# Kernel tuning notes

Hardware: AMD Instinct MI355X
Metric: run time of the kernel (lower is better)

The kernel has to match this reference:

```python
import jax, jax.numpy as jnp
import numpy as np

BN_EPS = 1e-5
COS_EPS = 1e-8


def _bn_train(x, gamma, beta):
    # BatchNorm1d in training mode: stats over (batch, length) per channel
    mean = jnp.mean(x, axis=(0, 2), keepdims=True)
    var = jnp.var(x, axis=(0, 2), keepdims=True)
    xn = (x - mean) * jax.lax.rsqrt(var + BN_EPS)
    return xn * gamma[None, :, None] + beta[None, :, None]


def _conv1d(x, w, pad):
    # x: [B, Cin, L], w: [Cout, Cin, K]
    return jax.lax.conv_general_dilated(
        x, w, window_strides=(1,), padding=[(pad, pad)],
        dimension_numbers=('NCH', 'OIH', 'NCH'))


def _spe_self_atten(h):
    # h: [B, c, L]; cosine-similarity attention over channels
    norms = jnp.sqrt(jnp.sum(h * h, axis=2))                 # [B, c]
    denom = jnp.maximum(norms[:, :, None] * norms[:, None, :], COS_EPS)
    sim = jnp.einsum('bcl,bdl->bcd', h, h) / denom            # [B, c, c]
    att = jax.nn.softmax(sim, axis=-1)
    return jnp.einsum('bcd,bdl->bcl', att, h) + h


def setup_inputs() -> dict:
    key = jax.random.key(0)
    ks = jax.random.split(key, 3)
    B, Cin, L = 256, 64, 2048
    planes, growth = 192, 48
    x = jax.random.normal(ks[0], (B, Cin, L), dtype=jnp.float32)
    W1 = jax.random.normal(ks[1], (planes, Cin, 1), dtype=jnp.float32) * (1.0 / np.sqrt(Cin))
    W2 = jax.random.normal(ks[2], (growth, planes, 3), dtype=jnp.float32) * (1.0 / np.sqrt(planes * 3))
    return {
        'x': x,
        'gamma1': jnp.ones((Cin,), jnp.float32),
        'beta1': jnp.zeros((Cin,), jnp.float32),
        'W1': W1,
        'gamma2': jnp.ones((planes,), jnp.float32),
        'beta2': jnp.zeros((planes,), jnp.float32),
        'W2': W2,
    }


def reference(x, gamma1, beta1, W1, gamma2, beta2, W2):
    out = jax.nn.relu(_bn_train(x, gamma1, beta1))
    out = _conv1d(out, W1, pad=0)
    out = jax.nn.relu(_bn_train(out, gamma2, beta2))
    out = _conv1d(out, W2, pad=1)
    out = _spe_self_atten(out)
    return jnp.concatenate((x, out), axis=1)
```

## Files before the change

### kernel.cpp

```cpp
#include <hip/hip_runtime.h>

#define BB 256
#define C0 64
#define LL 2048
#define PP 192
#define GG 48
#define CO 112
#define PBK 24
#define CBK 8

typedef float f32x4 __attribute__((ext_vector_type(4)));
typedef __bf16 bf16x8 __attribute__((ext_vector_type(8)));

static constexpr size_t OUT1_BYTES = (size_t)BB * PP * LL * 2;
static constexpr size_t H_BYTES    = (size_t)BB * GG * LL * 4;
static constexpr int    ZR_FLOATS  = 602624;

__device__ __forceinline__ float bflo(unsigned w) { return __uint_as_float(w << 16); }
__device__ __forceinline__ float bfhi(unsigned w) { return __uint_as_float(w & 0xffff0000u); }
__device__ __forceinline__ unsigned pk2bf(float a, float b) {
    unsigned ua = __float_as_uint(a); ua += 0x7fffu + ((ua >> 16) & 1u);
    unsigned ub = __float_as_uint(b); ub += 0x7fffu + ((ub >> 16) & 1u);
    return (ua >> 16) | (ub & 0xffff0000u);
}
__device__ __forceinline__ unsigned short f2bf(float f) {
    unsigned u = __float_as_uint(f); u += 0x7fffu + ((u >> 16) & 1u);
    return (unsigned short)(u >> 16);
}
__device__ __forceinline__ unsigned act2(unsigned w, float s0, float s1, float h0, float h1) {
    float y0 = fmaxf(fmaf(s0, bflo(w), h0), 0.f);
    float y1 = fmaxf(fmaf(s1, bfhi(w), h1), 0.f);
    return pk2bf(y0, y1);
}

__global__ void kp_pack(const float* __restrict__ W1, const float* __restrict__ W2,
                        unsigned short* __restrict__ W1p, unsigned short* __restrict__ W2p) {
    int i = blockIdx.x * 256 + threadIdx.x;
    if (i < PP * C0) W1p[i] = f2bf(W1[i]);
    if (i < 3 * GG * PP) {
        int tap = i / (GG * PP), r = i % (GG * PP);
        int g = r / PP, p = r % PP;
        W2p[i] = f2bf(W2[(g * PP + p) * 3 + tap]);
    }
}

__global__ __launch_bounds__(256) void k1_stats_copy_xT(
        const float* __restrict__ x, float* __restrict__ out, unsigned short* __restrict__ xT,
        float* __restrict__ bn1sum, float* __restrict__ bn1sq) {
    int b = blockIdx.x, lc = blockIdx.y, t = threadIdx.x;
    int c = t >> 2, li = t & 3;
    float s = 0.f, ss = 0.f;
    for (int q = 0; q < 16; ++q) {
        int l = lc * 256 + li * 64 + q * 4;
        float4 v = *(const float4*)&x[(size_t)(b * C0 + c) * LL + l];
        *(float4*)&out[(size_t)(b * CO + c) * LL + l] = v;
        s += v.x + v.y + v.z + v.w;
        ss += v.x * v.x + v.y * v.y + v.z * v.z + v.w * v.w;
        unsigned short* xp = &xT[(((size_t)(b * CBK + (c >> 3))) * LL + l) * 8 + (c & 7)];
        xp[0] = f2bf(v.x); xp[8] = f2bf(v.y); xp[16] = f2bf(v.z); xp[24] = f2bf(v.w);
    }
    s += __shfl_xor(s, 1); s += __shfl_xor(s, 2);
    ss += __shfl_xor(ss, 1); ss += __shfl_xor(ss, 2);
    if (li == 0) { atomicAdd(&bn1sum[c], s); atomicAdd(&bn1sq[c], ss); }
}

__global__ void k_bn_final(const float* __restrict__ sums, const float* __restrict__ sqs,
                           const float* __restrict__ gamma, const float* __restrict__ beta,
                           float* __restrict__ scale, float* __restrict__ shift,
                           int C, float invN) {
    int c = threadIdx.x;
    if (c < C) {
        float mean = sums[c] * invN;
        float var  = sqs[c] * invN - mean * mean;
        float r    = rsqrtf(var + 1e-5f);
        float sc   = gamma[c] * r;
        scale[c] = sc;
        shift[c] = beta[c] - mean * sc;
    }
}

__global__ __launch_bounds__(256, 2) void k2_conv1(
        const unsigned short* __restrict__ xT, const unsigned short* __restrict__ W1p,
        const float* __restrict__ par, unsigned short* __restrict__ out1) {
    int b = blockIdx.x, lt = blockIdx.y, t = threadIdx.x;
    int w = __builtin_amdgcn_readfirstlane(t >> 6);
    int lane = t & 63, lm = lane & 15, lg = lane >> 4;
    union AF { uint4 q; bf16x8 v; };
    AF afr[3][2];
    #pragma unroll
    for (int gf = 0; gf < 3; ++gf)
        #pragma unroll
        for (int kc = 0; kc < 2; ++kc)
            afr[gf][kc].q = *(const uint4*)&W1p[(w * 48 + gf * 16 + lm) * C0 + kc * 32 + lg * 8];
    f32x4 acc[3][8];
    #pragma unroll
    for (int gf = 0; gf < 3; ++gf)
        #pragma unroll
        for (int lf = 0; lf < 8; ++lf) acc[gf][lf] = f32x4{0.f, 0.f, 0.f, 0.f};
    int l0 = lt * 128;
    size_t xbase = (size_t)b * CBK * LL * 8;
    #pragma unroll
    for (int kc = 0; kc < 2; ++kc) {
        int cb = kc * 4 + lg;
        float4 sca = *(const float4*)&par[8 * cb];
        float4 scb = *(const float4*)&par[8 * cb + 4];
        float4 sha = *(const float4*)&par[64 + 8 * cb];
        float4 shb = *(const float4*)&par[64 + 8 * cb + 4];
        #pragma unroll
        for (int lf = 0; lf < 8; ++lf) {
            int l = l0 + lf * 16 + lm;
            uint4 q = *(const uint4*)&xT[xbase + ((size_t)cb * LL + l) * 8];
            union { uint4 q; bf16x8 v; } bf;
            bf.q.x = act2(q.x, sca.x, sca.y, sha.x, sha.y);
            bf.q.y = act2(q.y, sca.z, sca.w, sha.z, sha.w);
            bf.q.z = act2(q.z, scb.x, scb.y, shb.x, shb.y);
            bf.q.w = act2(q.w, scb.z, scb.w, shb.z, shb.w);
            #pragma unroll
            for (int gf = 0; gf < 3; ++gf)
                acc[gf][lf] = __builtin_amdgcn_mfma_f32_16x16x32_bf16(afr[gf][kc].v, bf.v, acc[gf][lf], 0, 0, 0);
        }
    }
    #pragma unroll
    for (int gf = 0; gf < 3; ++gf) {
        int g0 = w * 48 + gf * 16 + lg * 4;
        size_t obase = ((size_t)b * PBK + (g0 >> 3)) * LL * 8 + (g0 & 7);
        #pragma unroll
        for (int lf = 0; lf < 8; ++lf) {
            int l = l0 + lf * 16 + lm;
            uint2 pk;
            pk.x = pk2bf(acc[gf][lf][0], acc[gf][lf][1]);
            pk.y = pk2bf(acc[gf][lf][2], acc[gf][lf][3]);
            *(uint2*)&out1[obase + (size_t)l * 8] = pk;
        }
    }
}

__global__ __launch_bounds__(256) void k3_bn2_stats(
        const unsigned short* __restrict__ out1,
        float* __restrict__ bn2sum, float* __restrict__ bn2sq) {
    int pb = blockIdx.x, chunk = blockIdx.y, t = threadIdx.x;
    float s[8], ss[8];
    #pragma unroll
    for (int j = 0; j < 8; ++j) { s[j] = 0.f; ss[j] = 0.f; }
    for (int i = 0; i < 64; ++i) {
        int idx = chunk * 16384 + i * 256 + t;
        int b = idx >> 11, l = idx & 2047;
        uint4 q = *(const uint4*)&out1[(((size_t)(b * PBK + pb)) * LL + l) * 8];
        unsigned uu[4] = {q.x, q.y, q.z, q.w};
        #pragma unroll
        for (int j = 0; j < 4; ++j) {
            float f0 = bflo(uu[j]), f1 = bfhi(uu[j]);
            s[2 * j] += f0;      ss[2 * j] += f0 * f0;
            s[2 * j + 1] += f1;  ss[2 * j + 1] += f1 * f1;
        }
    }
    #pragma unroll
    for (int m = 1; m < 64; m <<= 1)
        #pragma unroll
        for (int j = 0; j < 8; ++j) { s[j] += __shfl_xor(s[j], m); ss[j] += __shfl_xor(ss[j], m); }
    if ((t & 63) == 0)
        #pragma unroll
        for (int j = 0; j < 8; ++j) {
            atomicAdd(&bn2sum[pb * 8 + j], s[j]);
            atomicAdd(&bn2sq[pb * 8 + j], ss[j]);
        }
}

__global__ __launch_bounds__(256, 2) void k4_conv2(
        const unsigned short* __restrict__ out1, const unsigned short* __restrict__ W2p,
        const float* __restrict__ par, float* __restrict__ h, float* __restrict__ norms2) {
    int b = blockIdx.x, lt = blockIdx.y, t = threadIdx.x;
    int w = __builtin_amdgcn_readfirstlane(t >> 6);
    int lane = t & 63, lm = lane & 15, lg = lane >> 4;
    int lb = lt * 128 + w * 32;
    f32x4 acc[3][2];
    #pragma unroll
    for (int gf = 0; gf < 3; ++gf) { acc[gf][0] = f32x4{0.f,0.f,0.f,0.f}; acc[gf][1] = f32x4{0.f,0.f,0.f,0.f}; }
    size_t obase = (size_t)b * PBK * LL * 8;
    for (int pc = 0; pc < 6; ++pc) {
        int pb = pc * 4 + lg;
        float4 sca = *(const float4*)&par[128 + 8 * pb];
        float4 scb = *(const float4*)&par[128 + 8 * pb + 4];
        float4 sha = *(const float4*)&par[320 + 8 * pb];
        float4 shb = *(const float4*)&par[320 + 8 * pb + 4];
        #pragma unroll
        for (int tap = 0; tap < 3; ++tap) {
            union AF { uint4 q; bf16x8 v; };
            AF afr[3];
            #pragma unroll
            for (int gf = 0; gf < 3; ++gf)
                afr[gf].q = *(const uint4*)&W2p[(tap * GG + gf * 16 + lm) * PP + pc * 32 + lg * 8];
            #pragma unroll
            for (int lf = 0; lf < 2; ++lf) {
                int lz = lb + lf * 16 + lm + tap - 1;
                union { uint4 q; bf16x8 v; } bf;
                if ((unsigned)lz < (unsigned)LL) {
                    uint4 q = *(const uint4*)&out1[obase + ((size_t)pb * LL + lz) * 8];
                    bf.q.x = act2(q.x, sca.x, sca.y, sha.x, sha.y);
                    bf.q.y = act2(q.y, sca.z, sca.w, sha.z, sha.w);
                    bf.q.z = act2(q.z, scb.x, scb.y, shb.x, shb.y);
                    bf.q.w = act2(q.w, scb.z, scb.w, shb.z, shb.w);
                } else {
                    bf.q = uint4{0u, 0u, 0u, 0u};
                }
                #pragma unroll
                for (int gf = 0; gf < 3; ++gf)
                    acc[gf][lf] = __builtin_amdgcn_mfma_f32_16x16x32_bf16(afr[gf].v, bf.v, acc[gf][lf], 0, 0, 0);
            }
        }
    }
    #pragma unroll
    for (int gf = 0; gf < 3; ++gf) {
        #pragma unroll
        for (int lf = 0; lf < 2; ++lf) {
            int l = lb + lf * 16 + lm;
            #pragma unroll
            for (int r = 0; r < 4; ++r) {
                int g = gf * 16 + lg * 4 + r;
                h[((size_t)(b * GG + g)) * LL + l] = acc[gf][lf][r];
            }
        }
        #pragma unroll
        for (int r = 0; r < 4; ++r) {
            float nv = acc[gf][0][r] * acc[gf][0][r] + acc[gf][1][r] * acc[gf][1][r];
            nv += __shfl_xor(nv, 1); nv += __shfl_xor(nv, 2);
            nv += __shfl_xor(nv, 4); nv += __shfl_xor(nv, 8);
            if (lm == 0) atomicAdd(&norms2[b * GG + gf * 16 + lg * 4 + r], nv);
        }
    }
}

__global__ __launch_bounds__(256) void k6_gram(
        const float* __restrict__ h, float* __restrict__ sim) {
    int b = blockIdx.x, ch = blockIdx.y, t = threadIdx.x;
    __shared__ float hl[GG * 260];
    int tr = t >> 4, tc = t & 15;
    float s00 = 0, s01 = 0, s02 = 0, s10 = 0, s11 = 0, s12 = 0, s20 = 0, s21 = 0, s22 = 0;
    for (int sub = 0; sub < 2; ++sub) {
        __syncthreads();
        for (int j = 0; j < 12; ++j) {
            int f = j * 256 + t;
            int r = f >> 6, lq = f & 63;
            float4 v = ((const float4*)h)[(size_t)(b * GG + r) * 512 + ch * 128 + sub * 64 + lq];
            *(float4*)&hl[r * 260 + lq * 4] = v;
        }
        __syncthreads();
        for (int l4 = 0; l4 < 64; ++l4) {
            float4 r0 = *(const float4*)&hl[(3 * tr + 0) * 260 + l4 * 4];
            float4 r1 = *(const float4*)&hl[(3 * tr + 1) * 260 + l4 * 4];
            float4 r2 = *(const float4*)&hl[(3 * tr + 2) * 260 + l4 * 4];
            float4 c0 = *(const float4*)&hl[(3 * tc + 0) * 260 + l4 * 4];
            float4 c1 = *(const float4*)&hl[(3 * tc + 1) * 260 + l4 * 4];
            float4 c2 = *(const float4*)&hl[(3 * tc + 2) * 260 + l4 * 4];
            s00 += r0.x * c0.x + r0.y * c0.y + r0.z * c0.z + r0.w * c0.w;
            s01 += r0.x * c1.x + r0.y * c1.y + r0.z * c1.z + r0.w * c1.w;
            s02 += r0.x * c2.x + r0.y * c2.y + r0.z * c2.z + r0.w * c2.w;
            s10 += r1.x * c0.x + r1.y * c0.y + r1.z * c0.z + r1.w * c0.w;
            s11 += r1.x * c1.x + r1.y * c1.y + r1.z * c1.z + r1.w * c1.w;
            s12 += r1.x * c2.x + r1.y * c2.y + r1.z * c2.z + r1.w * c2.w;
            s20 += r2.x * c0.x + r2.y * c0.y + r2.z * c0.z + r2.w * c0.w;
            s21 += r2.x * c1.x + r2.y * c1.y + r2.z * c1.z + r2.w * c1.w;
            s22 += r2.x * c2.x + r2.y * c2.y + r2.z * c2.z + r2.w * c2.w;
        }
    }
    float* sb = &sim[(size_t)b * 2304];
    atomicAdd(&sb[(3 * tr + 0) * 48 + 3 * tc + 0], s00);
    atomicAdd(&sb[(3 * tr + 0) * 48 + 3 * tc + 1], s01);
    atomicAdd(&sb[(3 * tr + 0) * 48 + 3 * tc + 2], s02);
    atomicAdd(&sb[(3 * tr + 1) * 48 + 3 * tc + 0], s10);
    atomicAdd(&sb[(3 * tr + 1) * 48 + 3 * tc + 1], s11);
    atomicAdd(&sb[(3 * tr + 1) * 48 + 3 * tc + 2], s12);
    atomicAdd(&sb[(3 * tr + 2) * 48 + 3 * tc + 0], s20);
    atomicAdd(&sb[(3 * tr + 2) * 48 + 3 * tc + 1], s21);
    atomicAdd(&sb[(3 * tr + 2) * 48 + 3 * tc + 2], s22);
}

__global__ __launch_bounds__(256) void k7_softmax_pv(
        const float* __restrict__ h, const float* __restrict__ sim,
        const float* __restrict__ norms2, float* __restrict__ out) {
    int b = blockIdx.x, ch = blockIdx.y, t = threadIdx.x;
    __shared__ float att[GG][GG];
    __shared__ float nrm[GG];
    if (t < GG) nrm[t] = sqrtf(norms2[b * GG + t]);
    __syncthreads();
    if (t < GG) {
        int r = t;
        const float* sr = &sim[(size_t)b * 2304 + r * 48];
        float nr = nrm[r];
        float m = -1e30f;
        for (int d = 0; d < GG; ++d) {
            float v = sr[d] / fmaxf(nr * nrm[d], 1e-8f);
            att[r][d] = v;
            m = fmaxf(m, v);
        }
        float ssum = 0.f;
        for (int d = 0; d < GG; ++d) {
            float e = __expf(att[r][d] - m);
            att[r][d] = e;
            ssum += e;
        }
        float inv = 1.f / ssum;
        for (int d = 0; d < GG; ++d) att[r][d] *= inv;
        att[r][r] += 1.0f;
    }
    __syncthreads();
    int l = ch * 512 + t;
    float h0[GG], h1[GG];
    #pragma unroll
    for (int d = 0; d < GG; ++d) {
        h0[d] = h[(size_t)(b * GG + d) * LL + l];
        h1[d] = h[(size_t)(b * GG + d) * LL + l + 256];
    }
    for (int c = 0; c < GG; ++c) {
        float a0 = 0.f, a1 = 0.f;
        #pragma unroll
        for (int dq = 0; dq < 12; ++dq) {
            float4 a4 = *(const float4*)&att[c][dq * 4];
            a0 += a4.x * h0[4 * dq] + a4.y * h0[4 * dq + 1] + a4.z * h0[4 * dq + 2] + a4.w * h0[4 * dq + 3];
            a1 += a4.x * h1[4 * dq] + a4.y * h1[4 * dq + 1] + a4.z * h1[4 * dq + 2] + a4.w * h1[4 * dq + 3];
        }
        out[(size_t)(b * CO + 64 + c) * LL + l] = a0;
        out[(size_t)(b * CO + 64 + c) * LL + l + 256] = a1;
    }
}

extern "C" void kernel_launch(void* const* d_in, const int* in_sizes, int n_in,
                              void* d_out, int out_size, void* d_ws, size_t ws_size,
                              hipStream_t stream) {
    const float* x      = (const float*)d_in[0];
    const float* gamma1 = (const float*)d_in[1];
    const float* beta1  = (const float*)d_in[2];
    const float* W1     = (const float*)d_in[3];
    const float* gamma2 = (const float*)d_in[4];
    const float* beta2  = (const float*)d_in[5];
    const float* W2     = (const float*)d_in[6];
    float* out = (float*)d_out;

    unsigned short* out1 = (unsigned short*)d_ws;
    float* h = (float*)((char*)d_ws + OUT1_BYTES);
    unsigned short* xT = (unsigned short*)h;
    float* zr  = (float*)((char*)d_ws + OUT1_BYTES + H_BYTES);
    float* par = zr + ZR_FLOATS;
    unsigned short* W1p = (unsigned short*)(par + 512);
    unsigned short* W2p = W1p + PP * C0;

    hipMemsetAsync(zr, 0, (size_t)ZR_FLOATS * sizeof(float), stream);

    const float invN = 1.0f / (float)((size_t)BB * LL);
    kp_pack<<<108, 256, 0, stream>>>(W1, W2, W1p, W2p);
    k1_stats_copy_xT<<<dim3(BB, 8), 256, 0, stream>>>(x, out, xT, zr + 0, zr + 64);
    k_bn_final<<<1, 64, 0, stream>>>(zr + 0, zr + 64, gamma1, beta1, par + 0, par + 64, 64, invN);
    k2_conv1<<<dim3(BB, 16), 256, 0, stream>>>(xT, W1p, par, out1);
    k3_bn2_stats<<<dim3(PBK, 32), 256, 0, stream>>>(out1, zr + 128, zr + 320);
    k_bn_final<<<1, 192, 0, stream>>>(zr + 128, zr + 320, gamma2, beta2, par + 128, par + 320, 192, invN);
    k4_conv2<<<dim3(BB, 16), 256, 0, stream>>>(out1, W2p, par, h, zr + 512);
    k6_gram<<<dim3(BB, 4), 256, 0, stream>>>(h, zr + 12800);
    k7_softmax_pv<<<dim3(BB, 4), 256, 0, stream>>>(h, zr + 12800, zr + 512, out);
}
```

Measured before the change: 839.6 us.

## Fuse BN2 stats into conv1, drop xT transpose, stage conv2 input in LDS

Removes the bf16 transposed copy of x. conv1 now reads fp32 x directly and applies BN1+ReLU on the fly. BN2 statistics are accumulated inside conv1 from the fp32 accumulators, so the separate stats pass over out1 is gone. Atomics are spread across 8 or 32 slots and reduced in bn_final. conv2 first stages the BN2+ReLU-activated tile, with its halo, in shared memory so the three taps reuse it instead of reloading global memory. It also switches to the hardware pack-to-bf16 instruction. The costs are strided scalar fp32 loads in conv1, and BN2 stats now come from unrounded fp32 values rather than the stored bf16.

```diff
diff --git a/kernel.cpp b/kernel.cpp
--- a/kernel.cpp
+++ b/kernel.cpp
@@ -7,21 +7,22 @@
 #define GG 48
 #define CO 112
 #define PBK 24
-#define CBK 8
 
 typedef float f32x4 __attribute__((ext_vector_type(4)));
 typedef __bf16 bf16x8 __attribute__((ext_vector_type(8)));
 
 static constexpr size_t OUT1_BYTES = (size_t)BB * PP * LL * 2;
 static constexpr size_t H_BYTES    = (size_t)BB * GG * LL * 4;
-static constexpr int    ZR_FLOATS  = 602624;
+static constexpr int ZR_FLOATS = 615424;
+static constexpr int ZO_BN1S = 0, ZO_BN1Q = 512, ZO_BN2S = 1024, ZO_BN2Q = 7168;
+static constexpr int ZO_NRM = 13312, ZO_SIM = 25600;
 
 __device__ __forceinline__ float bflo(unsigned w) { return __uint_as_float(w << 16); }
 __device__ __forceinline__ float bfhi(unsigned w) { return __uint_as_float(w & 0xffff0000u); }
 __device__ __forceinline__ unsigned pk2bf(float a, float b) {
-    unsigned ua = __float_as_uint(a); ua += 0x7fffu + ((ua >> 16) & 1u);
-    unsigned ub = __float_as_uint(b); ub += 0x7fffu + ((ub >> 16) & 1u);
-    return (ua >> 16) | (ub & 0xffff0000u);
+    unsigned r;
+    asm("v_cvt_pk_bf16_f32 %0, %1, %2" : "=v"(r) : "v"(a), "v"(b));
+    return r;
 }
 __device__ __forceinline__ unsigned short f2bf(float f) {
     unsigned u = __float_as_uint(f); u += 0x7fffu + ((u >> 16) & 1u);
@@ -44,34 +45,52 @@
     }
 }
 
-__global__ __launch_bounds__(256) void k1_stats_copy_xT(
-        const float* __restrict__ x, float* __restrict__ out, unsigned short* __restrict__ xT,
-        float* __restrict__ bn1sum, float* __restrict__ bn1sq) {
+__global__ __launch_bounds__(256) void k1_stats_copy(
+        const float* __restrict__ x, float* __restrict__ out,
+        float* __restrict__ bn1s, float* __restrict__ bn1q) {
     int b = blockIdx.x, lc = blockIdx.y, t = threadIdx.x;
-    int c = t >> 2, li = t & 3;
-    float s = 0.f, ss = 0.f;
-    for (int q = 0; q < 16; ++q) {
-        int l = lc * 256 + li * 64 + q * 4;
-        float4 v = *(const float4*)&x[(size_t)(b * C0 + c) * LL + l];
-        *(float4*)&out[(size_t)(b * CO + c) * LL + l] = v;
-        s += v.x + v.y + v.z + v.w;
-        ss += v.x * v.x + v.y * v.y + v.z * v.z + v.w * v.w;
-        unsigned short* xp = &xT[(((size_t)(b * CBK + (c >> 3))) * LL + l) * 8 + (c & 7)];
-        xp[0] = f2bf(v.x); xp[8] = f2bf(v.y); xp[16] = f2bf(v.z); xp[24] = f2bf(v.w);
-    }
-    s += __shfl_xor(s, 1); s += __shfl_xor(s, 2);
-    ss += __shfl_xor(ss, 1); ss += __shfl_xor(ss, 2);
-    if (li == 0) { atomicAdd(&bn1sum[c], s); atomicAdd(&bn1sq[c], ss); }
-}
-
-__global__ void k_bn_final(const float* __restrict__ sums, const float* __restrict__ sqs,
+    int lane = t & 63, w = t >> 6;
+    const float4* x4 = (const float4*)x;
+    float4* o4 = (float4*)out;
+    float s[16], q[16];
+    #pragma unroll
+    for (int it = 0; it < 16; ++it) { s[it] = 0.f; q[it] = 0.f; }
+    #pragma unroll
+    for (int it = 0; it < 16; ++it) {
+        int c = w + 4 * it;
+        #pragma unroll
+        for (int j = 0; j < 2; ++j) {
+            size_t idx = (size_t)(b * C0 + c) * 512 + lc * 128 + j * 64 + lane;
+            float4 v = x4[idx];
+            o4[(size_t)(b * CO + c) * 512 + lc * 128 + j * 64 + lane] = v;
+            s[it] += v.x + v.y + v.z + v.w;
+            q[it] += v.x * v.x + v.y * v.y + v.z * v.z + v.w * v.w;
+        }
+    }
+    #pragma unroll
+    for (int it = 0; it < 16; ++it) {
+        float a = s[it], d = q[it];
+        #pragma unroll
+        for (int m = 1; m < 64; m <<= 1) { a += __shfl_xor(a, m); d += __shfl_xor(d, m); }
+        if (lane == 0) {
+            int c = w + 4 * it;
+            int sp = (b * 4 + lc) & 7;
+            atomicAdd(&bn1s[sp * C0 + c], a);
+            atomicAdd(&bn1q[sp * C0 + c], d);
+        }
+    }
+}
+
+__global__ void k_bn_final(const float* __restrict__ ss, const float* __restrict__ qq,
                            const float* __restrict__ gamma, const float* __restrict__ beta,
                            float* __restrict__ scale, float* __restrict__ shift,
-                           int C, float invN) {
+                           int C, int nspread, float invN) {
     int c = threadIdx.x;
     if (c < C) {
-        float mean = sums[c] * invN;
-        float var  = sqs[c] * invN - mean * mean;
+        float s = 0.f, q = 0.f;
+        for (int k = 0; k < nspread; ++k) { s += ss[k * C + c]; q += qq[k * C + c]; }
+        float mean = s * invN;
+        float var  = q * invN - mean * mean;
         float r    = rsqrtf(var + 1e-5f);
         float sc   = gamma[c] * r;
         scale[c] = sc;
@@ -79,12 +98,14 @@
     }
 }
 
-__global__ __launch_bounds__(256, 2) void k2_conv1(
-        const unsigned short* __restrict__ xT, const unsigned short* __restrict__ W1p,
-        const float* __restrict__ par, unsigned short* __restrict__ out1) {
+__global__ __launch_bounds__(256) void k2_conv1(
+        const float* __restrict__ x, const unsigned short* __restrict__ W1p,
+        const float* __restrict__ par, unsigned short* __restrict__ out1,
+        float* __restrict__ bn2s, float* __restrict__ bn2q) {
     int b = blockIdx.x, lt = blockIdx.y, t = threadIdx.x;
+    int lane = t & 63;
     int w = __builtin_amdgcn_readfirstlane(t >> 6);
-    int lane = t & 63, lm = lane & 15, lg = lane >> 4;
+    int lm = lane & 15, lg = lane >> 4;
     union AF { uint4 q; bf16x8 v; };
     AF afr[3][2];
     #pragma unroll
@@ -98,28 +119,30 @@
         #pragma unroll
         for (int lf = 0; lf < 8; ++lf) acc[gf][lf] = f32x4{0.f, 0.f, 0.f, 0.f};
     int l0 = lt * 128;
-    size_t xbase = (size_t)b * CBK * LL * 8;
     #pragma unroll
     for (int kc = 0; kc < 2; ++kc) {
-        int cb = kc * 4 + lg;
-        float4 sca = *(const float4*)&par[8 * cb];
-        float4 scb = *(const float4*)&par[8 * cb + 4];
-        float4 sha = *(const float4*)&par[64 + 8 * cb];
-        float4 shb = *(const float4*)&par[64 + 8 * cb + 4];
+        int c0 = kc * 32 + lg * 8;
+        float sc[8], sh[8];
+        #pragma unroll
+        for (int j = 0; j < 8; ++j) { sc[j] = par[c0 + j]; sh[j] = par[64 + c0 + j]; }
         #pragma unroll
         for (int lf = 0; lf < 8; ++lf) {
             int l = l0 + lf * 16 + lm;
-            uint4 q = *(const uint4*)&xT[xbase + ((size_t)cb * LL + l) * 8];
+            float yv[8];
+            #pragma unroll
+            for (int j = 0; j < 8; ++j)
+                yv[j] = fmaxf(fmaf(sc[j], x[(size_t)(b * C0 + c0 + j) * LL + l], sh[j]), 0.f);
             union { uint4 q; bf16x8 v; } bf;
-            bf.q.x = act2(q.x, sca.x, sca.y, sha.x, sha.y);
-            bf.q.y = act2(q.y, sca.z, sca.w, sha.z, sha.w);
-            bf.q.z = act2(q.z, scb.x, scb.y, shb.x, shb.y);
-            bf.q.w = act2(q.w, scb.z, scb.w, shb.z, shb.w);
+            bf.q.x = pk2bf(yv[0], yv[1]); bf.q.y = pk2bf(yv[2], yv[3]);
+            bf.q.z = pk2bf(yv[4], yv[5]); bf.q.w = pk2bf(yv[6], yv[7]);
             #pragma unroll
             for (int gf = 0; gf < 3; ++gf)
                 acc[gf][lf] = __builtin_amdgcn_mfma_f32_16x16x32_bf16(afr[gf][kc].v, bf.v, acc[gf][lf], 0, 0, 0);
         }
     }
+    float s12[12], q12[12];
+    #pragma unroll
+    for (int i = 0; i < 12; ++i) { s12[i] = 0.f; q12[i] = 0.f; }
     #pragma unroll
     for (int gf = 0; gf < 3; ++gf) {
         int g0 = w * 48 + gf * 16 + lg * 4;
@@ -131,58 +154,79 @@
             pk.x = pk2bf(acc[gf][lf][0], acc[gf][lf][1]);
             pk.y = pk2bf(acc[gf][lf][2], acc[gf][lf][3]);
             *(uint2*)&out1[obase + (size_t)l * 8] = pk;
-        }
-    }
-}
-
-__global__ __launch_bounds__(256) void k3_bn2_stats(
-        const unsigned short* __restrict__ out1,
-        float* __restrict__ bn2sum, float* __restrict__ bn2sq) {
-    int pb = blockIdx.x, chunk = blockIdx.y, t = threadIdx.x;
-    float s[8], ss[8];
-    #pragma unroll
-    for (int j = 0; j < 8; ++j) { s[j] = 0.f; ss[j] = 0.f; }
-    for (int i = 0; i < 64; ++i) {
-        int idx = chunk * 16384 + i * 256 + t;
-        int b = idx >> 11, l = idx & 2047;
-        uint4 q = *(const uint4*)&out1[(((size_t)(b * PBK + pb)) * LL + l) * 8];
-        unsigned uu[4] = {q.x, q.y, q.z, q.w};
-        #pragma unroll
-        for (int j = 0; j < 4; ++j) {
-            float f0 = bflo(uu[j]), f1 = bfhi(uu[j]);
-            s[2 * j] += f0;      ss[2 * j] += f0 * f0;
-            s[2 * j + 1] += f1;  ss[2 * j + 1] += f1 * f1;
-        }
-    }
-    #pragma unroll
-    for (int m = 1; m < 64; m <<= 1)
-        #pragma unroll
-        for (int j = 0; j < 8; ++j) { s[j] += __shfl_xor(s[j], m); ss[j] += __shfl_xor(ss[j], m); }
-    if ((t & 63) == 0)
-        #pragma unroll
-        for (int j = 0; j < 8; ++j) {
-            atomicAdd(&bn2sum[pb * 8 + j], s[j]);
-            atomicAdd(&bn2sq[pb * 8 + j], ss[j]);
-        }
-}
-
-__global__ __launch_bounds__(256, 2) void k4_conv2(
+            #pragma unroll
+            for (int r = 0; r < 4; ++r) {
+                float v = acc[gf][lf][r];
+                s12[gf * 4 + r] += v;
+                q12[gf * 4 + r] = fmaf(v, v, q12[gf * 4 + r]);
+            }
+        }
+    }
+    int sp = (blockIdx.x * 16 + blockIdx.y) & 31;
+    #pragma unroll
+    for (int i = 0; i < 12; ++i) {
+        float a = s12[i], d = q12[i];
+        #pragma unroll
+        for (int m = 1; m < 16; m <<= 1) { a += __shfl_xor(a, m); d += __shfl_xor(d, m); }
+        if (lm == 0) {
+            int g = w * 48 + (i >> 2) * 16 + lg * 4 + (i & 3);
+            atomicAdd(&bn2s[sp * PP + g], a);
+            atomicAdd(&bn2q[sp * PP + g], d);
+        }
+    }
+}
+
+__global__ __launch_bounds__(256) void k4_conv2(
         const unsigned short* __restrict__ out1, const unsigned short* __restrict__ W2p,
         const float* __restrict__ par, float* __restrict__ h, float* __restrict__ norms2) {
     int b = blockIdx.x, lt = blockIdx.y, t = threadIdx.x;
+    __shared__ unsigned short zl[PBK * 130 * 8];
+    const float* sc2 = par + 128;
+    const float* sh2 = par + 320;
+    int l0 = lt * 128;
+    #pragma unroll
+    for (int j = 0; j < 12; ++j) {
+        int f = j * 256 + t;
+        int pb = f >> 7, fl = f & 127;
+        uint4 qv = *(const uint4*)&out1[(((size_t)(b * PBK + pb)) * LL + l0 + fl) * 8];
+        float4 sa = *(const float4*)&sc2[pb * 8];
+        float4 sb = *(const float4*)&sc2[pb * 8 + 4];
+        float4 ha = *(const float4*)&sh2[pb * 8];
+        float4 hb = *(const float4*)&sh2[pb * 8 + 4];
+        uint4 z;
+        z.x = act2(qv.x, sa.x, sa.y, ha.x, ha.y);
+        z.y = act2(qv.y, sa.z, sa.w, ha.z, ha.w);
+        z.z = act2(qv.z, sb.x, sb.y, hb.x, hb.y);
+        z.w = act2(qv.w, sb.z, sb.w, hb.z, hb.w);
+        *(uint4*)&zl[(pb * 130 + 1 + fl) * 8] = z;
+    }
+    if (t < 48) {
+        int pb = t >> 1, side = t & 1;
+        int li = side ? 129 : 0;
+        int l = l0 - 1 + li;
+        uint4 z = uint4{0u, 0u, 0u, 0u};
+        if ((unsigned)l < (unsigned)LL) {
+            uint4 qv = *(const uint4*)&out1[(((size_t)(b * PBK + pb)) * LL + l) * 8];
+            float4 sa = *(const float4*)&sc2[pb * 8];
+            float4 sb = *(const float4*)&sc2[pb * 8 + 4];
+            float4 ha = *(const float4*)&sh2[pb * 8];
+            float4 hb = *(const float4*)&sh2[pb * 8 + 4];
+            z.x = act2(qv.x, sa.x, sa.y, ha.x, ha.y);
+            z.y = act2(qv.y, sa.z, sa.w, ha.z, ha.w);
+            z.z = act2(qv.z, sb.x, sb.y, hb.x, hb.y);
+            z.w = act2(qv.w, sb.z, sb.w, hb.z, hb.w);
+        }
+        *(uint4*)&zl[(pb * 130 + li) * 8] = z;
+    }
+    __syncthreads();
+    int lane = t & 63;
     int w = __builtin_amdgcn_readfirstlane(t >> 6);
-    int lane = t & 63, lm = lane & 15, lg = lane >> 4;
-    int lb = lt * 128 + w * 32;
+    int lm = lane & 15, lg = lane >> 4;
     f32x4 acc[3][2];
     #pragma unroll
     for (int gf = 0; gf < 3; ++gf) { acc[gf][0] = f32x4{0.f,0.f,0.f,0.f}; acc[gf][1] = f32x4{0.f,0.f,0.f,0.f}; }
-    size_t obase = (size_t)b * PBK * LL * 8;
     for (int pc = 0; pc < 6; ++pc) {
         int pb = pc * 4 + lg;
-        float4 sca = *(const float4*)&par[128 + 8 * pb];
-        float4 scb = *(const float4*)&par[128 + 8 * pb + 4];
-        float4 sha = *(const float4*)&par[320 + 8 * pb];
-        float4 shb = *(const float4*)&par[320 + 8 * pb + 4];
         #pragma unroll
         for (int tap = 0; tap < 3; ++tap) {
             union AF { uint4 q; bf16x8 v; };
@@ -192,23 +236,15 @@
                 afr[gf].q = *(const uint4*)&W2p[(tap * GG + gf * 16 + lm) * PP + pc * 32 + lg * 8];
             #pragma unroll
             for (int lf = 0; lf < 2; ++lf) {
-                int lz = lb + lf * 16 + lm + tap - 1;
-                union { uint4 q; bf16x8 v; } bf;
-                if ((unsigned)lz < (unsigned)LL) {
-                    uint4 q = *(const uint4*)&out1[obase + ((size_t)pb * LL + lz) * 8];
-                    bf.q.x = act2(q.x, sca.x, sca.y, sha.x, sha.y);
-                    bf.q.y = act2(q.y, sca.z, sca.w, sha.z, sha.w);
-                    bf.q.z = act2(q.z, scb.x, scb.y, shb.x, shb.y);
-                    bf.q.w = act2(q.w, scb.z, scb.w, shb.z, shb.w);
-                } else {
-                    bf.q = uint4{0u, 0u, 0u, 0u};
-                }
+                int li = w * 32 + lf * 16 + lm + tap;
+                bf16x8 bv = *(const bf16x8*)&zl[(pb * 130 + li) * 8];
                 #pragma unroll
                 for (int gf = 0; gf < 3; ++gf)
-                    acc[gf][lf] = __builtin_amdgcn_mfma_f32_16x16x32_bf16(afr[gf].v, bf.v, acc[gf][lf], 0, 0, 0);
+                    acc[gf][lf] = __builtin_amdgcn_mfma_f32_16x16x32_bf16(afr[gf].v, bv, acc[gf][lf], 0, 0, 0);
             }
         }
     }
+    int lb = l0 + w * 32;
     #pragma unroll
     for (int gf = 0; gf < 3; ++gf) {
         #pragma unroll
@@ -337,8 +373,7 @@
     float* out = (float*)d_out;
 
     unsigned short* out1 = (unsigned short*)d_ws;
-    float* h = (float*)((char*)d_ws + OUT1_BYTES);
-    unsigned short* xT = (unsigned short*)h;
+    float* h   = (float*)((char*)d_ws + OUT1_BYTES);
     float* zr  = (float*)((char*)d_ws + OUT1_BYTES + H_BYTES);
     float* par = zr + ZR_FLOATS;
     unsigned short* W1p = (unsigned short*)(par + 512);
@@ -348,12 +383,13 @@
 
     const float invN = 1.0f / (float)((size_t)BB * LL);
     kp_pack<<<108, 256, 0, stream>>>(W1, W2, W1p, W2p);
-    k1_stats_copy_xT<<<dim3(BB, 8), 256, 0, stream>>>(x, out, xT, zr + 0, zr + 64);
-    k_bn_final<<<1, 64, 0, stream>>>(zr + 0, zr + 64, gamma1, beta1, par + 0, par + 64, 64, invN);
-    k2_conv1<<<dim3(BB, 16), 256, 0, stream>>>(xT, W1p, par, out1);
-    k3_bn2_stats<<<dim3(PBK, 32), 256, 0, stream>>>(out1, zr + 128, zr + 320);
-    k_bn_final<<<1, 192, 0, stream>>>(zr + 128, zr + 320, gamma2, beta2, par + 128, par + 320, 192, invN);
-    k4_conv2<<<dim3(BB, 16), 256, 0, stream>>>(out1, W2p, par, h, zr + 512);
-    k6_gram<<<dim3(BB, 4), 256, 0, stream>>>(h, zr + 12800);
-    k7_softmax_pv<<<dim3(BB, 4), 256, 0, stream>>>(h, zr + 12800, zr + 512, out);
-}
+    k1_stats_copy<<<dim3(BB, 4), 256, 0, stream>>>(x, out, zr + ZO_BN1S, zr + ZO_BN1Q);
+    k_bn_final<<<1, 64, 0, stream>>>(zr + ZO_BN1S, zr + ZO_BN1Q, gamma1, beta1,
+                                     par + 0, par + 64, C0, 8, invN);
+    k2_conv1<<<dim3(BB, 16), 256, 0, stream>>>(x, W1p, par, out1, zr + ZO_BN2S, zr + ZO_BN2Q);
+    k_bn_final<<<1, 192, 0, stream>>>(zr + ZO_BN2S, zr + ZO_BN2Q, gamma2, beta2,
+                                      par + 128, par + 320, PP, 32, invN);
+    k4_conv2<<<dim3(BB, 16), 256, 0, stream>>>(out1, W2p, par, h, zr + ZO_NRM);
+    k6_gram<<<dim3(BB, 4), 256, 0, stream>>>(h, zr + ZO_SIM);
+    k7_softmax_pv<<<dim3(BB, 4), 256, 0, stream>>>(h, zr + ZO_SIM, zr + ZO_NRM, out);
+}
```

Result: no change. 848.1 us (+1.0%).
